# Kernel tuning notes

Measured on AMD Instinct MI355X. Metric: run time of the kernel, lower is better.

The kernel has to match this reference:

```python
import jax, jax.numpy as jnp
import numpy as np

B, S, H, R = 32, 1024, 1024, 53
EPS = 1e-12
ATT_EPS = 1e10


def setup_inputs() -> dict:
    key = jax.random.key(0)
    ks = jax.random.split(key, 20)
    sc = 0.02
    n = lambda k, shape: jax.random.normal(k, shape, jnp.float32) * sc
    return {
        "relation": jax.random.randint(ks[0], (B, 1), 0, R),
        "last_hidden_size": jax.random.normal(ks[1], (B, S, H), jnp.float32),
        "sub_head": jax.random.randint(ks[2], (B, 1), 0, S),
        "sub_tail": jax.random.randint(ks[3], (B, 1), 0, S),
        "attention_mask": jax.random.randint(ks[4], (B, S), 0, 2).astype(jnp.int32),
        # learned params
        "rel_emb": n(ks[5], (R, H)),
        "Wrf": n(ks[6], (H, H)), "brf": jnp.zeros((H,), jnp.float32),
        "cln_w": jnp.ones((H,), jnp.float32), "cln_b": jnp.zeros((H,), jnp.float32),
        "Wwd": n(ks[7], (H, 2 * H)), "Wbd": n(ks[8], (H, 2 * H)),
        "Wq": n(ks[9], (H, H)), "bq": jnp.zeros((H,), jnp.float32),
        "Wk": n(ks[10], (H, H)), "bk": jnp.zeros((H,), jnp.float32),
        "Wv": n(ks[11], (H, H)), "bv": jnp.zeros((H,), jnp.float32),
        "Wo": n(ks[12], (1, H)), "bo": jnp.zeros((1,), jnp.float32),
    }


def reference(relation, last_hidden_size, sub_head, sub_tail, attention_mask,
              rel_emb, Wrf, brf, cln_w, cln_b, Wwd, Wbd,
              Wq, bq, Wk, bk, Wv, bv, Wo, bo):
    x = last_hidden_size  # [B,S,H]; dropout is identity at inference
    # relation feature: embedding -> linear -> ReLU6
    rel = jnp.clip(jnp.einsum('boh,gh->bog', rel_emb[relation], Wrf) + brf, 0.0, 6.0)  # [B,1,H]
    # gather subject head/tail token features
    bidx = jnp.arange(x.shape[0])[:, None]
    sub = (x[bidx, sub_head] + x[bidx, sub_tail]) * 0.5  # [B,1,H]
    cond = jnp.concatenate([rel, sub], axis=-1)  # [B,1,2H]
    # conditional layer norm: per-example weight/bias generated from cond
    w = jnp.einsum('boc,gc->bog', cond, Wwd) + cln_w  # [B,1,H]
    b = jnp.einsum('boc,gc->bog', cond, Wbd) + cln_b  # [B,1,H]
    mean = jnp.mean(x, axis=-1, keepdims=True)
    c = x - mean
    var = jnp.mean(c * c, axis=-1, keepdims=True)
    normed = c / jnp.sqrt(var + EPS) * w + b  # [B,S,H]
    # ReLU-activated QKV attention with additive mask bias and residual
    q = jax.nn.relu(jnp.einsum('bsh,gh->bsg', normed, Wq) + bq)
    k = jax.nn.relu(jnp.einsum('bsh,gh->bsg', normed, Wk) + bk)
    v = jax.nn.relu(jnp.einsum('bsh,gh->bsg', normed, Wv) + bv)
    e = jnp.einsum('bsh,bth->bst', q, k)  # [B,S,S]
    m = attention_mask.astype(e.dtype)[:, None, :]  # [B,1,S]
    e = e - ATT_EPS * (1.0 - m)
    a = jax.nn.softmax(e, axis=-1)
    hidden = jnp.einsum('bst,bth->bsh', a, v) + normed  # [B,S,H]
    pred_obj_head = (jnp.einsum('bsh,gh->bsg', hidden, Wo) + bo)[..., 0]  # [B,S]
    return (pred_obj_head, hidden)
```

## Files before the change

kernel.cpp:

```cpp
#include <hip/hip_runtime.h>
#include <hip/hip_bf16.h>

#define NB 32
#define NS 1024
#define NH 1024

typedef short s16x4 __attribute__((ext_vector_type(4)));
typedef short s16x8 __attribute__((ext_vector_type(8)));
typedef float f32x4 __attribute__((ext_vector_type(4)));

typedef __attribute__((address_space(3))) void lds_void;
typedef const __attribute__((address_space(1))) void gmem_void;

__device__ __forceinline__ short f2bf(float f) {
  __hip_bfloat16 h = __float2bfloat16(f);
  return *reinterpret_cast<short*>(&h);
}
__device__ __forceinline__ float bf2f(short s) {
  union { unsigned u; float f; } cv;
  cv.u = ((unsigned)(unsigned short)s) << 16;
  return cv.f;
}

__device__ __forceinline__ float wave_reduce_sum(float v) {
#pragma unroll
  for (int o = 32; o; o >>= 1) v += __shfl_xor(v, o);
  return v;
}
__device__ __forceinline__ float wave_reduce_max(float v) {
#pragma unroll
  for (int o = 32; o; o >>= 1) v = fmaxf(v, __shfl_xor(v, o));
  return v;
}
__device__ __forceinline__ float block_reduce_sum(float v, float* red) {
  v = wave_reduce_sum(v);
  __syncthreads();
  if ((threadIdx.x & 63) == 0) red[threadIdx.x >> 6] = v;
  __syncthreads();
  return red[0] + red[1] + red[2] + red[3];
}
__device__ __forceinline__ float block_reduce_max(float v, float* red) {
  v = wave_reduce_max(v);
  __syncthreads();
  if ((threadIdx.x & 63) == 0) red[threadIdx.x >> 6] = v;
  __syncthreads();
  return fmaxf(fmaxf(red[0], red[1]), fmaxf(red[2], red[3]));
}


#define BAR1 do { __builtin_amdgcn_s_barrier();                              \
                  asm volatile("s_waitcnt lgkmcnt(0)" ::: "memory");         \
                  __builtin_amdgcn_sched_barrier(0); } while (0)
#define BAR2 do { __builtin_amdgcn_s_barrier();                              \
                  asm volatile("" ::: "memory"); } while (0)
#define VW   asm volatile("s_waitcnt vmcnt(4)" ::: "memory")

#define GEMM_PRE()                                                           \
  __shared__ short lds[65536];                                               \
  const int tid  = threadIdx.x;                                              \
  const int lane = tid & 63;                                                 \
  const int w    = tid >> 6;                                                 \
  const int wm   = w >> 2, wn = w & 3;                                       \
  const int fr   = lane & 15, fq = lane >> 4;                                \
           \
  const long tA  = (long)(tid >> 3) * 1024 +                                 \
                   (((tid & 7) ^ ((tid >> 3) & 7)) << 3);                    \
                     \
  const int kc0  = (fq * 8) ^ ((fr & 7) * 8);                                \
  const int kc1  = (fq * 8 + 32) ^ ((fr & 7) * 8);                           \
  const int rdA  = wm * 8192 + fr * 64;                                      \
  const int rdB  = 16384 + (wn >> 1) * 8192 + (wn & 1) * 4096 + fr * 64;     \
  const int wsl  = w * 512;                                                  \
  f32x4 acc[8][4];                                                           \
  s16x8 aF[4][2], bF[2][2][2];                                               \
  _Pragma("unroll") for (int i_ = 0; i_ < 8; ++i_)                           \
    _Pragma("unroll") for (int j_ = 0; j_ < 4; ++j_)                         \
      acc[i_][j_] = (f32x4){0.f, 0.f, 0.f, 0.f};

#define STAGE(d, isB, h, kt)                                                 \
  do {                                                                       \
    const short* _g = ((isB) ? gB + (n0 + (h) * 128) * 1024                  \
                             : gA + (m0 + (h) * 128) * 1024) +               \
                      (long)((kt) & 15) * 64 + tA;                           \
    short* _l = lds + (d) * 32768 + (isB) * 16384 + (h) * 8192 + wsl;        \
    __builtin_amdgcn_global_load_lds((gmem_void*)_g, (lds_void*)_l,          \
                                     16, 0, 0);                              \
    __builtin_amdgcn_global_load_lds((gmem_void*)(_g + 65536),               \
                                     (lds_void*)(_l + 4096), 16, 0, 0);      \
  } while (0)

#define RD_A(d, mq)                                                          \
  _Pragma("unroll") for (int mi = 0; mi < 4; ++mi) {                         \
    aF[mi][0] = *(const s16x8*)(lds + (d) * 32768 + rdA + (mq) * 4096 +      \
                                mi * 1024 + kc0);                            \
    aF[mi][1] = *(const s16x8*)(lds + (d) * 32768 + rdA + (mq) * 4096 +      \
                                mi * 1024 + kc1);                            \
  }
#define RD_B(d, nq)                                                          \
  _Pragma("unroll") for (int ni = 0; ni < 2; ++ni) {                         \
    bF[nq][ni][0] = *(const s16x8*)(lds + (d) * 32768 + rdB + (nq) * 2048 +  \
                                    ni * 1024 + kc0);                        \
    bF[nq][ni][1] = *(const s16x8*)(lds + (d) * 32768 + rdB + (nq) * 2048 +  \
                                    ni * 1024 + kc1);                        \
  }
#define MMA(mq, nq)                                                          \
  do {                                                                       \
    __builtin_amdgcn_s_setprio(1);                                           \
    _Pragma("unroll") for (int kk = 0; kk < 2; ++kk)                         \
      _Pragma("unroll") for (int mi = 0; mi < 4; ++mi)                       \
        _Pragma("unroll") for (int ni = 0; ni < 2; ++ni)                     \
          acc[(mq) * 4 + mi][(nq) * 2 + ni] =                                \
              __builtin_amdgcn_mfma_f32_16x16x32_bf16(                       \
                  aF[mi][kk], bF[nq][ni][kk],                                \
                  acc[(mq) * 4 + mi][(nq) * 2 + ni], 0, 0, 0);               \
    __builtin_amdgcn_s_setprio(0);                                           \
  } while (0)

#define GEMM_MAIN()                                                          \
  GEMM_PRE();                                                                \
  STAGE(0, 1, 0, 0); STAGE(0, 1, 1, 0); STAGE(0, 0, 0, 0); STAGE(0, 0, 1, 0);\
  STAGE(1, 1, 0, 1); STAGE(1, 1, 1, 1);                                      \
  VW; BAR2;                                                                  \
  for (int it = 0; it < 8; ++it) {                                           \
    const int t1 = 2 * it + 1, t2 = 2 * it + 2, t3 = 2 * it + 3;             \
    RD_A(0, 0); RD_B(0, 0); STAGE(1, 0, 0, t1); BAR1; MMA(0, 0); BAR2;       \
    RD_B(0, 1);             STAGE(1, 0, 1, t1); BAR1; MMA(0, 1); BAR2;       \
    RD_A(0, 1);             STAGE(0, 1, 0, t2); BAR1; MMA(1, 1); BAR2;       \
                            STAGE(0, 1, 1, t2); BAR1; MMA(1, 0); VW; BAR2;   \
    RD_A(1, 0); RD_B(1, 0); STAGE(0, 0, 0, t2); BAR1; MMA(0, 0); BAR2;       \
    RD_B(1, 1);             STAGE(0, 0, 1, t2); BAR1; MMA(0, 1); BAR2;       \
    RD_A(1, 1);             STAGE(1, 1, 0, t3); BAR1; MMA(1, 1); BAR2;       \
                            STAGE(1, 1, 1, t3); BAR1; MMA(1, 0); VW; BAR2;   \
  }


__global__ __launch_bounds__(256) void cvtw_kernel(const float* __restrict__ Wq,
    const float* __restrict__ Wk, const float* __restrict__ Wv, short* __restrict__ out) {
  long i = ((long)blockIdx.x * 256 + threadIdx.x) * 4;
  int seg = (int)(i >> 20);
  long off = i & 1048575;
  const float* src = seg == 0 ? Wq : (seg == 1 ? Wk : Wv);
  f32x4 v = *(const f32x4*)(src + off);
  s16x4 o = { f2bf(v[0]), f2bf(v[1]), f2bf(v[2]), f2bf(v[3]) };
  *(s16x4*)(out + i) = o;
}

__global__ __launch_bounds__(256) void cond_kernel(const int* __restrict__ relation,
    const float* __restrict__ x, const int* __restrict__ sub_head,
    const int* __restrict__ sub_tail, const float* __restrict__ rel_emb,
    const float* __restrict__ Wrf, const float* __restrict__ brf, float* __restrict__ cond) {
  const int b = blockIdx.x;
  const int gc = blockIdx.y;
  const int tid = threadIdx.x;
  __shared__ float r[NH];
  const int rid = relation[b];
  for (int h = tid * 4; h < NH; h += 1024)
    *(f32x4*)(r + h) = *(const f32x4*)(rel_emb + (long)rid * NH + h);
  if (gc == 0) {
    const int sh = sub_head[b], st = sub_tail[b];
    for (int h = tid * 4; h < NH; h += 1024) {
      f32x4 a = *(const f32x4*)(x + ((long)b * NS + sh) * NH + h);
      f32x4 c = *(const f32x4*)(x + ((long)b * NS + st) * NH + h);
      f32x4 o = { 0.5f * (a[0] + c[0]), 0.5f * (a[1] + c[1]),
                  0.5f * (a[2] + c[2]), 0.5f * (a[3] + c[3]) };
      *(f32x4*)(cond + b * 2 * NH + NH + h) = o;
    }
  }
  __syncthreads();
  const int lane = tid & 63, wid = tid >> 6;
#pragma unroll
  for (int gi = 0; gi < 16; ++gi) {
    const int g = gc * 64 + wid * 16 + gi;
    float s = 0.f;
#pragma unroll
    for (int h = lane * 4; h < NH; h += 256) {
      f32x4 wv = *(const f32x4*)(Wrf + (long)g * NH + h);
      f32x4 rv = *(const f32x4*)(r + h);
      s += wv[0] * rv[0] + wv[1] * rv[1] + wv[2] * rv[2] + wv[3] * rv[3];
    }
    s = wave_reduce_sum(s);
    if (lane == 0) cond[b * 2 * NH + g] = fminf(fmaxf(s + brf[g], 0.f), 6.f);
  }
}

__global__ __launch_bounds__(256) void wb_kernel(const float* __restrict__ cond,
    const float* __restrict__ Wwd, const float* __restrict__ Wbd,
    const float* __restrict__ cln_w, const float* __restrict__ cln_b,
    float* __restrict__ wln, float* __restrict__ bln) {
  const int g = blockIdx.x;
  const int tid = threadIdx.x;
  __shared__ float wrow[2 * NH];
  __shared__ float brow[2 * NH];
  for (int i = tid * 4; i < 2 * NH; i += 1024) {
    *(f32x4*)(wrow + i) = *(const f32x4*)(Wwd + (long)g * 2 * NH + i);
    *(f32x4*)(brow + i) = *(const f32x4*)(Wbd + (long)g * 2 * NH + i);
  }
  __syncthreads();
  const int lane = tid & 63, wid = tid >> 6;
  const float cw = cln_w[g], cb = cln_b[g];
  for (int b = wid; b < NB; b += 4) {
    float sw = 0.f, sb = 0.f;
#pragma unroll
    for (int c = lane * 4; c < 2 * NH; c += 256) {
      f32x4 cv = *(const f32x4*)(cond + b * 2 * NH + c);
      f32x4 wv = *(const f32x4*)(wrow + c);
      f32x4 bv = *(const f32x4*)(brow + c);
      sw += cv[0] * wv[0] + cv[1] * wv[1] + cv[2] * wv[2] + cv[3] * wv[3];
      sb += cv[0] * bv[0] + cv[1] * bv[1] + cv[2] * bv[2] + cv[3] * bv[3];
    }
    sw = wave_reduce_sum(sw);
    sb = wave_reduce_sum(sb);
    if (lane == 0) {
      wln[b * NH + g] = sw + cw;
      bln[b * NH + g] = sb + cb;
    }
  }
}

__global__ __launch_bounds__(256) void ln_kernel(const float* __restrict__ x,
    const float* __restrict__ wln, const float* __restrict__ bln, short* __restrict__ normed) {
  const long row = blockIdx.x;
  const int tid = threadIdx.x;
  const long b = row >> 10;
  __shared__ float red[4];
  f32x4 v = *(const f32x4*)(x + row * NH + tid * 4);
  float mean = block_reduce_sum(v[0] + v[1] + v[2] + v[3], red) * (1.f / NH);
  float c0 = v[0] - mean, c1 = v[1] - mean, c2 = v[2] - mean, c3 = v[3] - mean;
  float var = block_reduce_sum(c0 * c0 + c1 * c1 + c2 * c2 + c3 * c3, red) * (1.f / NH);
  float rstd = rsqrtf(var + 1e-12f);
  f32x4 wv = *(const f32x4*)(wln + b * NH + tid * 4);
  f32x4 bv = *(const f32x4*)(bln + b * NH + tid * 4);
  s16x4 o = { f2bf(c0 * rstd * wv[0] + bv[0]), f2bf(c1 * rstd * wv[1] + bv[1]),
              f2bf(c2 * rstd * wv[2] + bv[2]), f2bf(c3 * rstd * wv[3] + bv[3]) };
  *(s16x4*)(normed + row * NH + tid * 4) = o;
}

__global__ __launch_bounds__(512, 2) void qkv_kernel(const short* __restrict__ A,
    const short* __restrict__ Wqb, const short* __restrict__ Wkb, const short* __restrict__ Wvb,
    const float* __restrict__ bq, const float* __restrict__ bk, const float* __restrict__ bv,
    short* __restrict__ q, short* __restrict__ k, short* __restrict__ vT) {
  const int z = blockIdx.z;
  const short* gA = A;
  const short* gB = z == 0 ? Wqb : (z == 1 ? Wkb : Wvb);
  const float* bias = z == 0 ? bq : (z == 1 ? bk : bv);
  const long m0 = (long)blockIdx.x * 256;
  const long n0 = (long)blockIdx.y * 256;
  GEMM_MAIN();
#pragma unroll
  for (int mI = 0; mI < 8; ++mI)
#pragma unroll
    for (int nI = 0; nI < 4; ++nI) {
      const long col = n0 + wn * 64 + nI * 16 + fr;
      const float bcol = bias[col];
#pragma unroll
      for (int r = 0; r < 4; ++r) {
        const long row = m0 + wm * 128 + mI * 16 + fq * 4 + r;
        float val = fmaxf(acc[mI][nI][r] + bcol, 0.f);
        short sv = f2bf(val);
        if (z == 0)      q[row * NH + col] = sv;
        else if (z == 1) k[row * NH + col] = sv;
        else             vT[((row >> 10) * NH + col) * NS + (row & 1023)] = sv;
      }
    }
}

__global__ __launch_bounds__(512, 2) void escore_kernel(const short* __restrict__ q,
    const short* __restrict__ k, const int* __restrict__ amask, float* __restrict__ e) {
  const int b = blockIdx.z;
  const short* gA = q + (long)b * NS * NH;
  const short* gB = k + (long)b * NS * NH;
  const long m0 = (long)blockIdx.x * 256;
  const long n0 = (long)blockIdx.y * 256;
  GEMM_MAIN();
  float* eb = e + (long)b * NS * NS;
#pragma unroll
  for (int mI = 0; mI < 8; ++mI)
#pragma unroll
    for (int nI = 0; nI < 4; ++nI) {
      const long col = n0 + wn * 64 + nI * 16 + fr;
      const float mb = -1e10f * (1.f - (float)amask[b * NS + col]);
#pragma unroll
      for (int r = 0; r < 4; ++r) {
        const long row = m0 + wm * 128 + mI * 16 + fq * 4 + r;
        eb[row * NS + col] = acc[mI][nI][r] + mb;
      }
    }
}

__global__ __launch_bounds__(256) void softmax_kernel(const float* __restrict__ e,
    short* __restrict__ a, float* __restrict__ inv_sum) {
  const long row = blockIdx.x;
  const int tid = threadIdx.x;
  __shared__ float red[4];
  f32x4 v = *(const f32x4*)(e + row * NS + tid * 4);
  float m = block_reduce_max(fmaxf(fmaxf(v[0], v[1]), fmaxf(v[2], v[3])), red);
  float p0 = expf(v[0] - m), p1 = expf(v[1] - m);
  float p2 = expf(v[2] - m), p3 = expf(v[3] - m);
  float s = block_reduce_sum(p0 + p1 + p2 + p3, red);
  s16x4 o = { f2bf(p0), f2bf(p1), f2bf(p2), f2bf(p3) };
  *(s16x4*)(a + row * NS + tid * 4) = o;
  if (tid == 0) inv_sum[row] = 1.f / s;
}

__global__ __launch_bounds__(512, 2) void av_kernel(const short* __restrict__ a,
    const short* __restrict__ vT, const float* __restrict__ inv_sum,
    const short* __restrict__ normed, float* __restrict__ hid) {
  const int b = blockIdx.z;
  const short* gA = a + (long)b * NS * NS;
  const short* gB = vT + (long)b * NH * NS;
  const long m0 = (long)blockIdx.x * 256;
  const long n0 = (long)blockIdx.y * 256;
  GEMM_MAIN();
#pragma unroll
  for (int mI = 0; mI < 8; ++mI)
#pragma unroll
    for (int nI = 0; nI < 4; ++nI) {
      const long col = n0 + wn * 64 + nI * 16 + fr;
#pragma unroll
      for (int r = 0; r < 4; ++r) {
        const long row = m0 + wm * 128 + mI * 16 + fq * 4 + r;
        const long gi = ((long)b * NS + row) * NH + col;
        hid[gi] = acc[mI][nI][r] * inv_sum[b * NS + row] + bf2f(normed[gi]);
      }
    }
}

__global__ __launch_bounds__(256) void pred_kernel(const float* __restrict__ hid,
    const float* __restrict__ Wo, const float* __restrict__ bo, float* __restrict__ pred) {
  const int row = blockIdx.x * 4 + (threadIdx.x >> 6);
  const int lane = threadIdx.x & 63;
  const float* hr = hid + (long)row * NH;
  float s = 0.f;
#pragma unroll
  for (int i = 0; i < 4; ++i) {
    f32x4 hv = *(const f32x4*)(hr + i * 256 + lane * 4);
    f32x4 wv = *(const f32x4*)(Wo + i * 256 + lane * 4);
    s += hv[0] * wv[0] + hv[1] * wv[1] + hv[2] * wv[2] + hv[3] * wv[3];
  }
  s = wave_reduce_sum(s);
  if (lane == 0) pred[row] = s + bo[0];
}

extern "C" void kernel_launch(void* const* d_in, const int* in_sizes, int n_in,
                              void* d_out, int out_size, void* d_ws, size_t ws_size,
                              hipStream_t stream) {
  (void)in_sizes; (void)n_in; (void)out_size; (void)ws_size;
  const int*   relation = (const int*)d_in[0];
  const float* x        = (const float*)d_in[1];
  const int*   sub_head = (const int*)d_in[2];
  const int*   sub_tail = (const int*)d_in[3];
  const int*   amask    = (const int*)d_in[4];
  const float* rel_emb  = (const float*)d_in[5];
  const float* Wrf      = (const float*)d_in[6];
  const float* brf      = (const float*)d_in[7];
  const float* cln_w    = (const float*)d_in[8];
  const float* cln_b    = (const float*)d_in[9];
  const float* Wwd      = (const float*)d_in[10];
  const float* Wbd      = (const float*)d_in[11];
  const float* Wq       = (const float*)d_in[12];
  const float* bq       = (const float*)d_in[13];
  const float* Wk       = (const float*)d_in[14];
  const float* bk       = (const float*)d_in[15];
  const float* Wv       = (const float*)d_in[16];
  const float* bv       = (const float*)d_in[17];
  const float* Wo       = (const float*)d_in[18];
  const float* bo       = (const float*)d_in[19];

  char* ws = (char*)d_ws;
  short* wq_bf = (short*)ws;
  short* wk_bf = wq_bf + 1048576;
  short* wv_bf = wk_bf + 1048576;
  float* cond    = (float*)(ws + 6291456);
  float* wln     = cond + 32 * 2048;
  float* bln     = wln + 32 * 1024;
  float* inv_sum = bln + 32 * 1024;
  short* normed  = (short*)(inv_sum + 32768);
  short* qb      = normed + 33554432;
  short* kb      = qb + 33554432;
  short* vT      = kb + 33554432;
  float* e       = (float*)(vT + 33554432);

  float* pred = (float*)d_out;
  float* hid  = pred + 32768;

  cvtw_kernel<<<3072, 256, 0, stream>>>(Wq, Wk, Wv, wq_bf);
  cond_kernel<<<dim3(NB, 16), 256, 0, stream>>>(relation, x, sub_head, sub_tail,
                                                rel_emb, Wrf, brf, cond);
  wb_kernel<<<NH, 256, 0, stream>>>(cond, Wwd, Wbd, cln_w, cln_b, wln, bln);
  ln_kernel<<<NB * NS, 256, 0, stream>>>(x, wln, bln, normed);
  qkv_kernel<<<dim3(128, 4, 3), 512, 0, stream>>>(normed, wq_bf, wk_bf, wv_bf,
                                                  bq, bk, bv, qb, kb, vT);
  escore_kernel<<<dim3(4, 4, 32), 512, 0, stream>>>(qb, kb, amask, e);
  softmax_kernel<<<NB * NS, 256, 0, stream>>>(e, qb, inv_sum);
  av_kernel<<<dim3(4, 4, 32), 512, 0, stream>>>(qb, vT, inv_sum, normed, hid);
  pred_kernel<<<NB * NS / 4, 256, 0, stream>>>(hid, Wo, bo, pred);
}
```

Measured before the change: 581.9 us.

## Coalesce V-transpose via LDS, reorder QKV grid, fuse output projection into AV

The QKV GEMM now treats the three weight matrices as one concatenated N=3072 matrix, with the grid reordered so N tiles vary fastest, which lets consecutive blocks reuse the same A rows. The V output is staged through padded LDS and written transposed with 16-byte vector stores instead of strided scalar stores. The separate pred kernel, which re-read all of hid, is removed: the AV epilogue accumulates per-row partial dot products with Wo, reduces them across lanes by shuffles, and a small finish kernel sums 16 partials per row. This adds a partial-sum buffer and a larger LDS allocation in the QKV kernel.

```diff
diff --git a/kernel.cpp b/kernel.cpp
--- a/kernel.cpp
+++ b/kernel.cpp
@@ -56,7 +56,6 @@
 #define VW   asm volatile("s_waitcnt vmcnt(4)" ::: "memory")
 
 #define GEMM_PRE()                                                           \
-  __shared__ short lds[65536];                                               \
   const int tid  = threadIdx.x;                                              \
   const int lane = tid & 63;                                                 \
   const int w    = tid >> 6;                                                 \
@@ -236,36 +235,63 @@
 }
 
 __global__ __launch_bounds__(512, 2) void qkv_kernel(const short* __restrict__ A,
-    const short* __restrict__ Wqb, const short* __restrict__ Wkb, const short* __restrict__ Wvb,
+    const short* __restrict__ Wqkv,
     const float* __restrict__ bq, const float* __restrict__ bk, const float* __restrict__ bv,
     short* __restrict__ q, short* __restrict__ k, short* __restrict__ vT) {
-  const int z = blockIdx.z;
+  __shared__ short lds[67584];
   const short* gA = A;
-  const short* gB = z == 0 ? Wqb : (z == 1 ? Wkb : Wvb);
+  const short* gB = Wqkv;
+  const long n0 = (long)blockIdx.x * 256;
+  const long m0 = (long)blockIdx.y * 256;
+  GEMM_MAIN();
+  const int z = blockIdx.x >> 2;
+  const long hc0 = (long)(blockIdx.x & 3) * 256;
   const float* bias = z == 0 ? bq : (z == 1 ? bk : bv);
-  const long m0 = (long)blockIdx.x * 256;
-  const long n0 = (long)blockIdx.y * 256;
-  GEMM_MAIN();
-#pragma unroll
-  for (int mI = 0; mI < 8; ++mI)
+  if (z < 2) {
+    short* dst = z == 0 ? q : k;
 #pragma unroll
     for (int nI = 0; nI < 4; ++nI) {
-      const long col = n0 + wn * 64 + nI * 16 + fr;
+      const long col = hc0 + wn * 64 + nI * 16 + fr;
       const float bcol = bias[col];
 #pragma unroll
-      for (int r = 0; r < 4; ++r) {
-        const long row = m0 + wm * 128 + mI * 16 + fq * 4 + r;
-        float val = fmaxf(acc[mI][nI][r] + bcol, 0.f);
-        short sv = f2bf(val);
-        if (z == 0)      q[row * NH + col] = sv;
-        else if (z == 1) k[row * NH + col] = sv;
-        else             vT[((row >> 10) * NH + col) * NS + (row & 1023)] = sv;
+      for (int mI = 0; mI < 8; ++mI)
+#pragma unroll
+        for (int r = 0; r < 4; ++r) {
+          const long row = m0 + wm * 128 + mI * 16 + fq * 4 + r;
+          dst[row * NH + col] = f2bf(fmaxf(acc[mI][nI][r] + bcol, 0.f));
+        }
+    }
+  } else {
+    asm volatile("s_waitcnt vmcnt(0)" ::: "memory");
+    __syncthreads();
+#pragma unroll
+    for (int nI = 0; nI < 4; ++nI) {
+      const int hl = wn * 64 + nI * 16 + fr;
+      const float bcol = bias[hc0 + hl];
+#pragma unroll
+      for (int mI = 0; mI < 8; ++mI) {
+        const int tl = wm * 128 + mI * 16 + fq * 4;
+        s16x4 pk = { f2bf(fmaxf(acc[mI][nI][0] + bcol, 0.f)),
+                     f2bf(fmaxf(acc[mI][nI][1] + bcol, 0.f)),
+                     f2bf(fmaxf(acc[mI][nI][2] + bcol, 0.f)),
+                     f2bf(fmaxf(acc[mI][nI][3] + bcol, 0.f)) };
+        *(s16x4*)(lds + hl * 264 + tl) = pk;
       }
     }
+    __syncthreads();
+    const int h = tid >> 1, half = tid & 1;
+    const long bb = m0 >> 10;
+    short* dst = vT + ((bb * NH) + hc0 + h) * NS + (m0 & 1023) + half * 128;
+    const short* src = lds + h * 264 + half * 128;
+#pragma unroll
+    for (int j = 0; j < 16; ++j)
+      *(s16x8*)(dst + j * 8) = *(const s16x8*)(src + j * 8);
+  }
 }
 
 __global__ __launch_bounds__(512, 2) void escore_kernel(const short* __restrict__ q,
     const short* __restrict__ k, const int* __restrict__ amask, float* __restrict__ e) {
+  __shared__ short lds[65536];
   const int b = blockIdx.z;
   const short* gA = q + (long)b * NS * NH;
   const short* gB = k + (long)b * NS * NH;
@@ -304,41 +330,61 @@
 
 __global__ __launch_bounds__(512, 2) void av_kernel(const short* __restrict__ a,
     const short* __restrict__ vT, const float* __restrict__ inv_sum,
-    const short* __restrict__ normed, float* __restrict__ hid) {
+    const short* __restrict__ normed, const float* __restrict__ Wo,
+    float* __restrict__ hid, float* __restrict__ pred_part) {
+  __shared__ short lds[65536];
   const int b = blockIdx.z;
   const short* gA = a + (long)b * NS * NS;
   const short* gB = vT + (long)b * NH * NS;
   const long m0 = (long)blockIdx.x * 256;
   const long n0 = (long)blockIdx.y * 256;
   GEMM_MAIN();
+  float pp[8][4];
 #pragma unroll
   for (int mI = 0; mI < 8; ++mI)
 #pragma unroll
-    for (int nI = 0; nI < 4; ++nI) {
-      const long col = n0 + wn * 64 + nI * 16 + fr;
+    for (int r = 0; r < 4; ++r) pp[mI][r] = 0.f;
+#pragma unroll
+  for (int nI = 0; nI < 4; ++nI) {
+    const long col = n0 + wn * 64 + nI * 16 + fr;
+    const float wo = Wo[col];
+#pragma unroll
+    for (int mI = 0; mI < 8; ++mI)
 #pragma unroll
       for (int r = 0; r < 4; ++r) {
         const long row = m0 + wm * 128 + mI * 16 + fq * 4 + r;
         const long gi = ((long)b * NS + row) * NH + col;
-        hid[gi] = acc[mI][nI][r] * inv_sum[b * NS + row] + bf2f(normed[gi]);
+        float hv = acc[mI][nI][r] * inv_sum[b * NS + row] + bf2f(normed[gi]);
+        hid[gi] = hv;
+        pp[mI][r] += hv * wo;
       }
-    }
-}
-
-__global__ __launch_bounds__(256) void pred_kernel(const float* __restrict__ hid,
-    const float* __restrict__ Wo, const float* __restrict__ bo, float* __restrict__ pred) {
-  const int row = blockIdx.x * 4 + (threadIdx.x >> 6);
-  const int lane = threadIdx.x & 63;
-  const float* hr = hid + (long)row * NH;
-  float s = 0.f;
-#pragma unroll
-  for (int i = 0; i < 4; ++i) {
-    f32x4 hv = *(const f32x4*)(hr + i * 256 + lane * 4);
-    f32x4 wv = *(const f32x4*)(Wo + i * 256 + lane * 4);
-    s += hv[0] * wv[0] + hv[1] * wv[1] + hv[2] * wv[2] + hv[3] * wv[3];
-  }
-  s = wave_reduce_sum(s);
-  if (lane == 0) pred[row] = s + bo[0];
+  }
+#pragma unroll
+  for (int mI = 0; mI < 8; ++mI)
+#pragma unroll
+    for (int r = 0; r < 4; ++r) {
+      float v = pp[mI][r];
+      v += __shfl_xor(v, 1);
+      v += __shfl_xor(v, 2);
+      v += __shfl_xor(v, 4);
+      v += __shfl_xor(v, 8);
+      if (fr == 0)
+        pred_part[((long)blockIdx.y * 4 + wn) * (NB * NS) + (long)b * NS + m0 +
+                  wm * 128 + mI * 16 + fq * 4 + r] = v;
+    }
+}
+
+__global__ __launch_bounds__(256) void pred_finish_kernel(const float* __restrict__ pp,
+    const float* __restrict__ bo, float* __restrict__ pred) {
+  const int i = (blockIdx.x * 256 + threadIdx.x) * 4;
+  const float bz = bo[0];
+  f32x4 o = { bz, bz, bz, bz };
+#pragma unroll
+  for (int j = 0; j < 16; ++j) {
+    f32x4 a = *(const f32x4*)(pp + (long)j * (NB * NS) + i);
+    o[0] += a[0]; o[1] += a[1]; o[2] += a[2]; o[3] += a[3];
+  }
+  *(f32x4*)(pred + i) = o;
 }
 
 extern "C" void kernel_launch(void* const* d_in, const int* in_sizes, int n_in,
@@ -367,9 +413,7 @@
   const float* bo       = (const float*)d_in[19];
 
   char* ws = (char*)d_ws;
-  short* wq_bf = (short*)ws;
-  short* wk_bf = wq_bf + 1048576;
-  short* wv_bf = wk_bf + 1048576;
+  short* wqkv_bf = (short*)ws;
   float* cond    = (float*)(ws + 6291456);
   float* wln     = cond + 32 * 2048;
   float* bln     = wln + 32 * 1024;
@@ -379,19 +423,21 @@
   short* kb      = qb + 33554432;
   short* vT      = kb + 33554432;
   float* e       = (float*)(vT + 33554432);
+  float* pred_part = e + 33554432;
 
   float* pred = (float*)d_out;
   float* hid  = pred + 32768;
 
-  cvtw_kernel<<<3072, 256, 0, stream>>>(Wq, Wk, Wv, wq_bf);
+  cvtw_kernel<<<3072, 256, 0, stream>>>(Wq, Wk, Wv, wqkv_bf);
   cond_kernel<<<dim3(NB, 16), 256, 0, stream>>>(relation, x, sub_head, sub_tail,
                                                 rel_emb, Wrf, brf, cond);
   wb_kernel<<<NH, 256, 0, stream>>>(cond, Wwd, Wbd, cln_w, cln_b, wln, bln);
   ln_kernel<<<NB * NS, 256, 0, stream>>>(x, wln, bln, normed);
-  qkv_kernel<<<dim3(128, 4, 3), 512, 0, stream>>>(normed, wq_bf, wk_bf, wv_bf,
-                                                  bq, bk, bv, qb, kb, vT);
+  qkv_kernel<<<dim3(12, 128), 512, 0, stream>>>(normed, wqkv_bf,
+                                                bq, bk, bv, qb, kb, vT);
   escore_kernel<<<dim3(4, 4, 32), 512, 0, stream>>>(qb, kb, amask, e);
   softmax_kernel<<<NB * NS, 256, 0, stream>>>(e, qb, inv_sum);
-  av_kernel<<<dim3(4, 4, 32), 512, 0, stream>>>(qb, vT, inv_sum, normed, hid);
-  pred_kernel<<<NB * NS / 4, 256, 0, stream>>>(hid, Wo, bo, pred);
-}
+  av_kernel<<<dim3(4, 4, 32), 512, 0, stream>>>(qb, vT, inv_sum, normed, Wo,
+                                                hid, pred_part);
+  pred_finish_kernel<<<32, 256, 0, stream>>>(pred_part, bo, pred);
+}
```

After: 535.2 us. 8.0% less time.
